# Performance work log

Measured on AMD Instinct MI355X. Metric: run time of the kernel, lower is better.

Reference implementation:

```python
import jax, jax.numpy as jnp
import numpy as np


def log_g(x):
    # torch: where(x>=0, log(relu(x)+0.5), -softplus(-x))
    return jnp.where(x >= 0, jnp.log(jnp.maximum(x, 0.0) + 0.5), -jax.nn.softplus(-x))


def parallel_scan_log(log_coeffs, log_values):
    # Faithful to source: cumsum over LAST (feature) dim, then pad time dim
    # (axis=1) with one leading zero row; logcumsumexp over time dim (axis=1).
    a_star = jnp.cumsum(log_coeffs, axis=-1)                      # [B,T,D]
    a_star = jnp.pad(a_star, ((0, 0), (1, 0), (0, 0)))            # [B,T+1,D]
    log_h0_plus_b_star = jax.lax.cumlogsumexp(log_values - a_star, axis=1)
    return jnp.exp(a_star + log_h0_plus_b_star)                   # [B,T+1,D]


def setup_inputs() -> dict:
    key = jax.random.key(0)
    ks = jax.random.split(key, 8)
    B, T, Din, Dout = 8, 4096, 1024, 1024
    scale = 1.0 / np.sqrt(Din)
    return {
        "x": jax.random.normal(ks[0], (B, T, Din), dtype=jnp.float32),
        "h_0": jax.random.uniform(ks[1], (B, 1, Dout), dtype=jnp.float32),
        "Wi": jax.random.uniform(ks[2], (Dout, Din), jnp.float32, -scale, scale),
        "bi": jax.random.uniform(ks[3], (Dout,), jnp.float32, -scale, scale),
        "Wf": jax.random.uniform(ks[4], (Dout, Din), jnp.float32, -scale, scale),
        "bf": jax.random.uniform(ks[5], (Dout,), jnp.float32, -scale, scale),
        "Wh": jax.random.uniform(ks[6], (Dout, Din), jnp.float32, -scale, scale),
        "bh": jax.random.uniform(ks[7], (Dout,), jnp.float32, -scale, scale),
    }


def reference(x, h_0, Wi, bi, Wf, bf, Wh, bh):
    # gate pre-activations: [B,T,Dout]
    zi = jnp.einsum('btd,od->bto', x, Wi) + bi
    zf = jnp.einsum('btd,od->bto', x, Wf) + bf
    zh = jnp.einsum('btd,od->bto', x, Wh) + bh
    diff = jax.nn.softplus(-zf) - jax.nn.softplus(-zi)
    log_f = -jax.nn.softplus(diff)
    log_i = -jax.nn.softplus(-diff)
    log_values = jnp.concatenate([log_g(h_0), log_i + log_g(zh)], axis=1)  # [B,T+1,D]
    return parallel_scan_log(log_f, log_values)
```

## Files before the change

### kernel.cpp

```cpp
#include <hip/hip_runtime.h>
#include <math.h>
#include <stdint.h>

#define B_    8
#define T_    4096
#define TP1   4097
#define D_    1024
#define K_    1024
#define M_    32768

#define BLK_M 128
#define BLK_N 64
#define BK    32

#define TC    64
#define NC    65

typedef __attribute__((ext_vector_type(8))) _Float16 f16x8;
typedef __attribute__((ext_vector_type(4))) float    f32x4;

__device__ __forceinline__ float sp_f(float x) {
    return fmaxf(x, 0.0f) + __logf(1.0f + __expf(-fabsf(x)));
}
__device__ __forceinline__ float log_g_f(float x) {
    return (x >= 0.0f) ? __logf(x + 0.5f) : x - __logf(1.0f + __expf(x));
}

__device__ __forceinline__ void g2lds16(const void* g, void* l) {
    __builtin_amdgcn_global_load_lds(
        (const __attribute__((address_space(1))) uint32_t*)g,
        (__attribute__((address_space(3))) uint32_t*)l,
        16, 0, 0);
}

__global__ __launch_bounds__(256) void k_cvt_x(
    const float* __restrict__ X, _Float16* __restrict__ Xs)
{
    int g = blockIdx.x * 256 + threadIdx.x;
    int l = g & 63;
    int frag = g >> 6;
    int kt = frag & 31;
    int mt = frag >> 5;
    int m = (mt << 4) + (l & 15);
    int k = (kt << 5) + ((l >> 4) << 3);
    const float4* p = (const float4*)&X[(size_t)m * K_ + k];
    float4 a = p[0], b = p[1];
    f16x8 h;
    h[0]=(_Float16)a.x; h[1]=(_Float16)a.y; h[2]=(_Float16)a.z; h[3]=(_Float16)a.w;
    h[4]=(_Float16)b.x; h[5]=(_Float16)b.y; h[6]=(_Float16)b.z; h[7]=(_Float16)b.w;
    *(f16x8*)&Xs[(size_t)g * 8] = h;
}

__global__ __launch_bounds__(256) void k_cvt_w(
    const float* __restrict__ Wi, const float* __restrict__ Wf,
    const float* __restrict__ Wh, _Float16* __restrict__ Ws)
{
    int g = blockIdx.x * 256 + threadIdx.x;
    int mat = g >> 17;
    int r = g & 131071;
    const float* W = (mat == 0) ? Wi : (mat == 1) ? Wf : Wh;
    int l = r & 63;
    int frag = r >> 6;
    int kt = frag & 31;
    int nt = frag >> 5;
    int n = (nt << 4) + (l & 15);
    int k = (kt << 5) + ((l >> 4) << 3);
    const float4* p = (const float4*)&W[(size_t)n * K_ + k];
    float4 a = p[0], b = p[1];
    f16x8 h;
    h[0]=(_Float16)a.x; h[1]=(_Float16)a.y; h[2]=(_Float16)a.z; h[3]=(_Float16)a.w;
    h[4]=(_Float16)b.x; h[5]=(_Float16)b.y; h[6]=(_Float16)b.z; h[7]=(_Float16)b.w;
    *(f16x8*)&Ws[(size_t)g * 8] = h;
}

__device__ __forceinline__ void stage_tile(
    const _Float16* Ag, const _Float16* Bg, int kt,
    _Float16* lAbuf, _Float16* lBbuf, int fa0, int fb0)
{
    g2lds16(Ag + (size_t)(fa0 * 32 + kt) * 512,       lAbuf + fa0 * 512);
    g2lds16(Ag + (size_t)((fa0 + 1) * 32 + kt) * 512, lAbuf + (fa0 + 1) * 512);
#pragma unroll
    for (int j = 0; j < 3; ++j) {
        int fb  = fb0 + j;
        int mat = fb >> 2, nf = fb & 3;
        g2lds16(Bg + ((size_t)mat * 2048 + (size_t)nf * 32 + kt) * 512,
                lBbuf + fb * 512);
    }
}

__device__ __forceinline__ void compute_tile(
    const _Float16* lAbuf, const _Float16* lBbuf,
    int wm, int wnf, int lane, f32x4 acc[3][4][2])
{
    f16x8 af[4];
#pragma unroll
    for (int mt = 0; mt < 4; ++mt)
        af[mt] = *(const f16x8*)&lAbuf[((wm >> 4) + mt) * 512 + lane * 8];
    __builtin_amdgcn_s_setprio(1);
#pragma unroll
    for (int a = 0; a < 3; ++a) {
#pragma unroll
        for (int nt = 0; nt < 2; ++nt) {
            f16x8 bfr = *(const f16x8*)&lBbuf[(a * 4 + wnf + nt) * 512 + lane * 8];
#pragma unroll
            for (int mt = 0; mt < 4; ++mt)
                acc[a][mt][nt] = __builtin_amdgcn_mfma_f32_16x16x32_f16(
                    af[mt], bfr, acc[a][mt][nt], 0, 0, 0);
        }
    }
    __builtin_amdgcn_s_setprio(0);
}

#define WAITBAR(N) do {                                         \
    asm volatile("s_waitcnt vmcnt(" #N ")" ::: "memory");       \
    __builtin_amdgcn_s_barrier();                               \
} while (0)

__global__ __launch_bounds__(256) void k_gemm(
    const _Float16* __restrict__ Xs, const _Float16* __restrict__ Ws,
    const float* __restrict__ bi, const float* __restrict__ bfv,
    const float* __restrict__ bh,
    float* __restrict__ ws_a, float* __restrict__ out)
{
    __shared__ __align__(16) _Float16 lA[3][8 * 512];
    __shared__ __align__(16) _Float16 lB[3][12 * 512];

    const int tid  = threadIdx.x;
    const int lane = tid & 63;
    const int w    = tid >> 6;

    const int bid = blockIdx.y * (int)gridDim.x + blockIdx.x;
    const int cpx = ((int)gridDim.x * (int)gridDim.y) >> 3;
    const int swz = (bid & 7) * cpx + (bid >> 3);
    const int n0  = (swz & 15) * BLK_N;
    const int m0  = (swz >> 4) * BLK_M;

    const int wm   = (w >> 1) * 64;
    const int wnf  = (w & 1) * 2;
    const int l16  = lane & 15;
    const int q    = lane >> 4;

    const int fa0 = w * 2;
    const int fb0 = w * 3;

    const _Float16* Ag = Xs + ((size_t)(m0 >> 4) * 32) * 512 + (size_t)lane * 8;
    const _Float16* Bg = Ws + (size_t)(n0 >> 4) * 32 * 512 + (size_t)lane * 8;

    f32x4 acc[3][4][2];
#pragma unroll
    for (int a = 0; a < 3; ++a)
#pragma unroll
        for (int mt = 0; mt < 4; ++mt)
#pragma unroll
            for (int nt = 0; nt < 2; ++nt) acc[a][mt][nt] = (f32x4)(0.0f);

    stage_tile(Ag, Bg, 0, lA[0], lB[0], fa0, fb0);
    stage_tile(Ag, Bg, 1, lA[1], lB[1], fa0, fb0);
    WAITBAR(5);

    for (int it = 0; it < 10; ++it) {
        const int kt = it * 3;

        stage_tile(Ag, Bg, kt + 2, lA[2], lB[2], fa0, fb0);
        compute_tile(lA[0], lB[0], wm, wnf, lane, acc);
        WAITBAR(5);

        stage_tile(Ag, Bg, kt + 3, lA[0], lB[0], fa0, fb0);
        compute_tile(lA[1], lB[1], wm, wnf, lane, acc);
        WAITBAR(5);

        stage_tile(Ag, Bg, kt + 4, lA[1], lB[1], fa0, fb0);
        compute_tile(lA[2], lB[2], wm, wnf, lane, acc);
        WAITBAR(5);
    }
    compute_tile(lA[0], lB[0], wm, wnf, lane, acc);
    WAITBAR(0);
    compute_tile(lA[1], lB[1], wm, wnf, lane, acc);

#pragma unroll
    for (int mt = 0; mt < 4; ++mt) {
#pragma unroll
        for (int nt = 0; nt < 2; ++nt) {
            int n = n0 + (wnf + nt) * 16 + l16;
            float biv = bi[n], bfvv = bfv[n], bhv = bh[n];
#pragma unroll
            for (int r = 0; r < 4; ++r) {
                int m = m0 + wm + mt * 16 + q * 4 + r;
                float zi = acc[0][mt][nt][r] + biv;
                float zf = acc[1][mt][nt][r] + bfvv;
                float zh = acc[2][mt][nt][r] + bhv;
                float spf = fmaxf(-zf, 0.0f) + __logf(1.0f + __expf(-fabsf(zf)));
                float spi = fmaxf(-zi, 0.0f) + __logf(1.0f + __expf(-fabsf(zi)));
                float df  = spf - spi;
                float spd = fmaxf(df, 0.0f) + __logf(1.0f + __expf(-fabsf(df)));
                float lf  = -spd;
                float li  = df - spd;
                float lg  = (zh >= 0.0f) ? __logf(zh + 0.5f)
                                         : zh - __logf(1.0f + __expf(zh));
                float lv  = li + lg;
                ws_a[(size_t)m * D_ + n] = lf;
                int b = m >> 12;
                out[(size_t)(m + b + 1) * D_ + n] = lv;
            }
        }
    }
}

__global__ __launch_bounds__(256) void k_cumsum(
    float* __restrict__ ws_a, float* __restrict__ out)
{
    const int tid  = threadIdx.x;
    const int lane = tid & 63;
    const int row  = blockIdx.x * 4 + (tid >> 6);
    const int b    = row >> 12;
    float* pa = ws_a + (size_t)row * D_;
    float* pu = out + (size_t)(row + b + 1) * D_;

    float vals[16];
#pragma unroll
    for (int j = 0; j < 4; ++j) {
        float4 v = *(const float4*)&pa[lane * 16 + j * 4];
        vals[j*4+0] = v.x; vals[j*4+1] = v.y; vals[j*4+2] = v.z; vals[j*4+3] = v.w;
    }
    float s = 0.0f;
#pragma unroll
    for (int j = 0; j < 16; ++j) s += vals[j];
    float inc = s;
#pragma unroll
    for (int off = 1; off < 64; off <<= 1) {
        float nv = __shfl_up(inc, off);
        if (lane >= off) inc += nv;
    }
    float run = inc - s;
#pragma unroll
    for (int j = 0; j < 16; ++j) { run += vals[j]; vals[j] = run; }
#pragma unroll
    for (int j = 0; j < 4; ++j) {
        float4 lv4 = *(const float4*)&pu[lane * 16 + j * 4];
        float4 a4; a4.x = vals[j*4]; a4.y = vals[j*4+1]; a4.z = vals[j*4+2]; a4.w = vals[j*4+3];
        float4 u4; u4.x = lv4.x - a4.x; u4.y = lv4.y - a4.y;
                   u4.z = lv4.z - a4.z; u4.w = lv4.w - a4.w;
        *(float4*)&pa[lane * 16 + j * 4] = a4;
        *(float4*)&pu[lane * 16 + j * 4] = u4;
    }
}

__global__ void k_h0(const float* __restrict__ h0, float* __restrict__ out)
{
    int i = blockIdx.x * 256 + threadIdx.x;
    int b = i >> 10, d = i & 1023;
    out[(size_t)b * TP1 * D_ + d] = log_g_f(h0[i]);
}

__global__ __launch_bounds__(256) void k_chunk(
    const float* __restrict__ out, float* __restrict__ ctm, float* __restrict__ cts)
{
    int c = blockIdx.x, b = blockIdx.y;
    int d = threadIdx.x * 4;
    int t0 = c * TC, t1 = min(TP1, t0 + TC);
    float4 m = make_float4(-__builtin_inff(), -__builtin_inff(),
                           -__builtin_inff(), -__builtin_inff());
    float4 s = make_float4(0.f, 0.f, 0.f, 0.f);
    const float* p = out + ((size_t)b * TP1 + t0) * D_ + d;
    for (int t = t0; t < t1; ++t) {
        float4 u = *(const float4*)p; p += D_;
        float4 mn;
        mn.x = fmaxf(m.x, u.x); mn.y = fmaxf(m.y, u.y);
        mn.z = fmaxf(m.z, u.z); mn.w = fmaxf(m.w, u.w);
        s.x = s.x * __expf(m.x - mn.x) + __expf(u.x - mn.x);
        s.y = s.y * __expf(m.y - mn.y) + __expf(u.y - mn.y);
        s.z = s.z * __expf(m.z - mn.z) + __expf(u.z - mn.z);
        s.w = s.w * __expf(m.w - mn.w) + __expf(u.w - mn.w);
        m = mn;
    }
    int ci = (b * NC + c) * D_ + d;
    *(float4*)&ctm[ci] = m; *(float4*)&cts[ci] = s;
}

__global__ __launch_bounds__(256) void k_carry(
    const float* __restrict__ ctm, const float* __restrict__ cts,
    float* __restrict__ carry)
{
    int i = blockIdx.x * 256 + threadIdx.x;
    int b = i >> 10, d = i & 1023;
    float m = -__builtin_inff(), s = 0.0f;
    for (int c = 0; c < NC; ++c) {
        int ci = (b * NC + c) * D_ + d;
        carry[ci] = (s == 0.0f) ? -__builtin_inff() : (m + __logf(s));
        float m2 = ctm[ci], s2 = cts[ci];
        float M = fmaxf(m, m2);
        s = s * __expf(m - M) + s2 * __expf(m2 - M);
        m = M;
    }
}

__global__ __launch_bounds__(256) void k_final(
    const float* __restrict__ ws_a, const float* __restrict__ carry,
    float* __restrict__ out)
{
    int c = blockIdx.x, b = blockIdx.y;
    int d = threadIdx.x * 4;
    int t0 = c * TC, t1 = min(TP1, t0 + TC);
    float4 v = *(const float4*)&carry[(b * NC + c) * D_ + d];
    float4 m, s;
    m.x = v.x; s.x = (v.x == -__builtin_inff()) ? 0.f : 1.f;
    m.y = v.y; s.y = (v.y == -__builtin_inff()) ? 0.f : 1.f;
    m.z = v.z; s.z = (v.z == -__builtin_inff()) ? 0.f : 1.f;
    m.w = v.w; s.w = (v.w == -__builtin_inff()) ? 0.f : 1.f;
    for (int t = t0; t < t1; ++t) {
        size_t oi = ((size_t)b * TP1 + t) * D_ + d;
        float4 u = *(const float4*)&out[oi];
        float4 mn;
        mn.x = fmaxf(m.x, u.x); mn.y = fmaxf(m.y, u.y);
        mn.z = fmaxf(m.z, u.z); mn.w = fmaxf(m.w, u.w);
        s.x = s.x * __expf(m.x - mn.x) + __expf(u.x - mn.x);
        s.y = s.y * __expf(m.y - mn.y) + __expf(u.y - mn.y);
        s.z = s.z * __expf(m.z - mn.z) + __expf(u.z - mn.z);
        s.w = s.w * __expf(m.w - mn.w) + __expf(u.w - mn.w);
        m = mn;
        float4 a = make_float4(0.f, 0.f, 0.f, 0.f);
        if (t != 0) a = *(const float4*)&ws_a[((size_t)b * T_ + (t - 1)) * D_ + d];
        float4 o;
        o.x = __expf(a.x + mn.x) * s.x;
        o.y = __expf(a.y + mn.y) * s.y;
        o.z = __expf(a.z + mn.z) * s.z;
        o.w = __expf(a.w + mn.w) * s.w;
        *(float4*)&out[oi] = o;
    }
}

extern "C" void kernel_launch(void* const* d_in, const int* in_sizes, int n_in,
                              void* d_out, int out_size, void* d_ws, size_t ws_size,
                              hipStream_t stream)
{
    const float* X   = (const float*)d_in[0];
    const float* h0  = (const float*)d_in[1];
    const float* Wi  = (const float*)d_in[2];
    const float* bi  = (const float*)d_in[3];
    const float* Wf  = (const float*)d_in[4];
    const float* bfv = (const float*)d_in[5];
    const float* Wh  = (const float*)d_in[6];
    const float* bh  = (const float*)d_in[7];
    float* out  = (float*)d_out;

    char* wsb = (char*)d_ws;
    float*    ws_a = (float*)wsb;
    _Float16* Xs   = (_Float16*)(wsb + (size_t)M_ * D_ * 4);
    _Float16* Wsv  = (_Float16*)(wsb + (size_t)M_ * D_ * 4 + (size_t)M_ * K_ * 2);
    float* ctm   = (float*)(wsb + (size_t)M_ * D_ * 4);
    float* cts   = ctm + B_ * NC * D_;
    float* carry = cts + B_ * NC * D_;

    k_cvt_x<<<M_ * K_ / 8 / 256, 256, 0, stream>>>(X, Xs);
    k_cvt_w<<<3 * D_ * K_ / 8 / 256, 256, 0, stream>>>(Wi, Wf, Wh, Wsv);

    dim3 g1(D_ / BLK_N, M_ / BLK_M);
    k_gemm<<<g1, 256, 0, stream>>>(Xs, Wsv, bi, bfv, bh, ws_a, out);
    k_h0<<<32, 256, 0, stream>>>(h0, out);
    k_cumsum<<<M_ / 4, 256, 0, stream>>>(ws_a, out);
    k_chunk<<<dim3(NC, B_), 256, 0, stream>>>(out, ctm, cts);
    k_carry<<<32, 256, 0, stream>>>(ctm, cts, carry);
    k_final<<<dim3(NC, B_), 256, 0, stream>>>(ws_a, carry, out);
}
```

Measured before the change: 804.6 us.

## Simplify gate log-math, merge conversion kernels, fold h0 into carry scan

The gate epilogue now computes log_f and log_i from two exponentials and three logs, using log(1+e^-zi)/(1+e^-zi + 1+e^-zf), instead of nested softplus calls. The two fp16 conversion kernels are merged into one launch, and the h0 row is handled inside the carry kernel, which seeds the scan so chunks align to 64 timesteps. The chunk kernel keeps two interleaved log-sum-exp accumulators to expose more instruction-level parallelism. The new form of the gate math may overflow in __expf for large negative pre-activations, a risk the softplus form avoided.

Result: faster. 763.8 us (-5.1%).

```diff
diff --git a/kernel.cpp b/kernel.cpp
--- a/kernel.cpp
+++ b/kernel.cpp
@@ -13,17 +13,20 @@
 #define BLK_N 64
 #define BK    32
 
-#define TC    64
-#define NC    65
+#define CH    64
+#define NCH   64
 
 typedef __attribute__((ext_vector_type(8))) _Float16 f16x8;
 typedef __attribute__((ext_vector_type(4))) float    f32x4;
 
-__device__ __forceinline__ float sp_f(float x) {
-    return fmaxf(x, 0.0f) + __logf(1.0f + __expf(-fabsf(x)));
-}
 __device__ __forceinline__ float log_g_f(float x) {
     return (x >= 0.0f) ? __logf(x + 0.5f) : x - __logf(1.0f + __expf(x));
+}
+
+__device__ __forceinline__ void lse_upd(float& m, float& s, float u) {
+    float mn = fmaxf(m, u);
+    s = s * __expf(m - mn) + __expf(u - mn);
+    m = mn;
 }
 
 __device__ __forceinline__ void g2lds16(const void* g, void* l) {
@@ -33,44 +36,44 @@
         16, 0, 0);
 }
 
-__global__ __launch_bounds__(256) void k_cvt_x(
-    const float* __restrict__ X, _Float16* __restrict__ Xs)
-{
-    int g = blockIdx.x * 256 + threadIdx.x;
-    int l = g & 63;
-    int frag = g >> 6;
-    int kt = frag & 31;
-    int mt = frag >> 5;
-    int m = (mt << 4) + (l & 15);
-    int k = (kt << 5) + ((l >> 4) << 3);
-    const float4* p = (const float4*)&X[(size_t)m * K_ + k];
-    float4 a = p[0], b = p[1];
-    f16x8 h;
-    h[0]=(_Float16)a.x; h[1]=(_Float16)a.y; h[2]=(_Float16)a.z; h[3]=(_Float16)a.w;
-    h[4]=(_Float16)b.x; h[5]=(_Float16)b.y; h[6]=(_Float16)b.z; h[7]=(_Float16)b.w;
-    *(f16x8*)&Xs[(size_t)g * 8] = h;
-}
-
-__global__ __launch_bounds__(256) void k_cvt_w(
-    const float* __restrict__ Wi, const float* __restrict__ Wf,
-    const float* __restrict__ Wh, _Float16* __restrict__ Ws)
-{
-    int g = blockIdx.x * 256 + threadIdx.x;
-    int mat = g >> 17;
-    int r = g & 131071;
-    const float* W = (mat == 0) ? Wi : (mat == 1) ? Wf : Wh;
-    int l = r & 63;
-    int frag = r >> 6;
-    int kt = frag & 31;
-    int nt = frag >> 5;
-    int n = (nt << 4) + (l & 15);
-    int k = (kt << 5) + ((l >> 4) << 3);
-    const float4* p = (const float4*)&W[(size_t)n * K_ + k];
-    float4 a = p[0], b = p[1];
-    f16x8 h;
-    h[0]=(_Float16)a.x; h[1]=(_Float16)a.y; h[2]=(_Float16)a.z; h[3]=(_Float16)a.w;
-    h[4]=(_Float16)b.x; h[5]=(_Float16)b.y; h[6]=(_Float16)b.z; h[7]=(_Float16)b.w;
-    *(f16x8*)&Ws[(size_t)g * 8] = h;
+__global__ __launch_bounds__(256) void k_cvt(
+    const float* __restrict__ X, const float* __restrict__ Wi,
+    const float* __restrict__ Wf, const float* __restrict__ Wh,
+    _Float16* __restrict__ Xs, _Float16* __restrict__ Ws)
+{
+    int bid = blockIdx.x;
+    if (bid < 1536) {
+        int g = bid * 256 + threadIdx.x;
+        int mat = g >> 17;
+        int r = g & 131071;
+        const float* W = (mat == 0) ? Wi : (mat == 1) ? Wf : Wh;
+        int l = r & 63;
+        int frag = r >> 6;
+        int kt = frag & 31;
+        int nt = frag >> 5;
+        int n = (nt << 4) + (l & 15);
+        int k = (kt << 5) + ((l >> 4) << 3);
+        const float4* p = (const float4*)&W[(size_t)n * K_ + k];
+        float4 a = p[0], b = p[1];
+        f16x8 h;
+        h[0]=(_Float16)a.x; h[1]=(_Float16)a.y; h[2]=(_Float16)a.z; h[3]=(_Float16)a.w;
+        h[4]=(_Float16)b.x; h[5]=(_Float16)b.y; h[6]=(_Float16)b.z; h[7]=(_Float16)b.w;
+        *(f16x8*)&Ws[(size_t)g * 8] = h;
+    } else {
+        int g = (bid - 1536) * 256 + threadIdx.x;
+        int l = g & 63;
+        int frag = g >> 6;
+        int kt = frag & 31;
+        int mt = frag >> 5;
+        int m = (mt << 4) + (l & 15);
+        int k = (kt << 5) + ((l >> 4) << 3);
+        const float4* p = (const float4*)&X[(size_t)m * K_ + k];
+        float4 a = p[0], b = p[1];
+        f16x8 h;
+        h[0]=(_Float16)a.x; h[1]=(_Float16)a.y; h[2]=(_Float16)a.z; h[3]=(_Float16)a.w;
+        h[4]=(_Float16)b.x; h[5]=(_Float16)b.y; h[6]=(_Float16)b.z; h[7]=(_Float16)b.w;
+        *(f16x8*)&Xs[(size_t)g * 8] = h;
+    }
 }
 
 __device__ __forceinline__ void stage_tile(
@@ -189,15 +192,14 @@
                 float zi = acc[0][mt][nt][r] + biv;
                 float zf = acc[1][mt][nt][r] + bfvv;
                 float zh = acc[2][mt][nt][r] + bhv;
-                float spf = fmaxf(-zf, 0.0f) + __logf(1.0f + __expf(-fabsf(zf)));
-                float spi = fmaxf(-zi, 0.0f) + __logf(1.0f + __expf(-fabsf(zi)));
-                float df  = spf - spi;
-                float spd = fmaxf(df, 0.0f) + __logf(1.0f + __expf(-fabsf(df)));
-                float lf  = -spd;
-                float li  = df - spd;
-                float lg  = (zh >= 0.0f) ? __logf(zh + 0.5f)
-                                         : zh - __logf(1.0f + __expf(zh));
-                float lv  = li + lg;
+                float ei = __expf(-zi), ef = __expf(-zf);
+                float Pi = 1.0f + ei,  Pf = 1.0f + ef;
+                float lS = __logf(Pi + Pf);
+                float lf = __logf(Pi) - lS;
+                float li = __logf(Pf) - lS;
+                float lg = (zh >= 0.0f) ? __logf(zh + 0.5f)
+                                        : zh - __logf(1.0f + __expf(zh));
+                float lv = li + lg;
                 ws_a[(size_t)m * D_ + n] = lf;
                 int b = m >> 12;
                 out[(size_t)(m + b + 1) * D_ + n] = lv;
@@ -245,25 +247,80 @@
     }
 }
 
-__global__ void k_h0(const float* __restrict__ h0, float* __restrict__ out)
+__global__ __launch_bounds__(256) void k_chunk(
+    const float* __restrict__ out, float* __restrict__ ctm, float* __restrict__ cts)
+{
+    int c = blockIdx.x, b = blockIdx.y;
+    int d = threadIdx.x * 4;
+    const float* p = out + ((size_t)b * TP1 + 1 + c * CH) * D_ + d;
+    float m0[4], s0[4], m1[4], s1[4];
+#pragma unroll
+    for (int e = 0; e < 4; ++e) {
+        m0[e] = -__builtin_inff(); s0[e] = 0.0f;
+        m1[e] = -__builtin_inff(); s1[e] = 0.0f;
+    }
+#pragma unroll 4
+    for (int i = 0; i < CH; i += 2) {
+        float4 ua = *(const float4*)(p + (size_t)i * D_);
+        float4 ub = *(const float4*)(p + (size_t)(i + 1) * D_);
+        lse_upd(m0[0], s0[0], ua.x); lse_upd(m0[1], s0[1], ua.y);
+        lse_upd(m0[2], s0[2], ua.z); lse_upd(m0[3], s0[3], ua.w);
+        lse_upd(m1[0], s1[0], ub.x); lse_upd(m1[1], s1[1], ub.y);
+        lse_upd(m1[2], s1[2], ub.z); lse_upd(m1[3], s1[3], ub.w);
+    }
+    size_t ci = ((size_t)b * NCH + c) * D_ + d;
+    float4 M4, S4;
+    {
+        float M, S;
+#define MERGE(e, dst_m, dst_s)                                        \
+        M = fmaxf(m0[e], m1[e]);                                      \
+        S = s0[e] * __expf(m0[e] - M) + s1[e] * __expf(m1[e] - M);    \
+        dst_m = M; dst_s = S;
+        MERGE(0, M4.x, S4.x); MERGE(1, M4.y, S4.y);
+        MERGE(2, M4.z, S4.z); MERGE(3, M4.w, S4.w);
+#undef MERGE
+    }
+    *(float4*)&ctm[ci] = M4;
+    *(float4*)&cts[ci] = S4;
+}
+
+__global__ __launch_bounds__(256) void k_carry(
+    const float* __restrict__ h0, const float* __restrict__ ctm,
+    const float* __restrict__ cts, float* __restrict__ carry,
+    float* __restrict__ out)
 {
     int i = blockIdx.x * 256 + threadIdx.x;
     int b = i >> 10, d = i & 1023;
-    out[(size_t)b * TP1 * D_ + d] = log_g_f(h0[i]);
-}
-
-__global__ __launch_bounds__(256) void k_chunk(
-    const float* __restrict__ out, float* __restrict__ ctm, float* __restrict__ cts)
+    float u0 = log_g_f(h0[i]);
+    out[(size_t)b * TP1 * D_ + d] = __expf(u0);
+    float m = u0, s = 1.0f;
+#pragma unroll 4
+    for (int c = 0; c < NCH; ++c) {
+        size_t ci = ((size_t)b * NCH + c) * D_ + d;
+        carry[ci] = m + __logf(s);
+        float m2 = ctm[ci], s2 = cts[ci];
+        float M = fmaxf(m, m2);
+        s = s * __expf(m - M) + s2 * __expf(m2 - M);
+        m = M;
+    }
+}
+
+__global__ __launch_bounds__(256) void k_final(
+    const float* __restrict__ ws_a, const float* __restrict__ carry,
+    float* __restrict__ out)
 {
     int c = blockIdx.x, b = blockIdx.y;
     int d = threadIdx.x * 4;
-    int t0 = c * TC, t1 = min(TP1, t0 + TC);
-    float4 m = make_float4(-__builtin_inff(), -__builtin_inff(),
-                           -__builtin_inff(), -__builtin_inff());
-    float4 s = make_float4(0.f, 0.f, 0.f, 0.f);
-    const float* p = out + ((size_t)b * TP1 + t0) * D_ + d;
-    for (int t = t0; t < t1; ++t) {
-        float4 u = *(const float4*)p; p += D_;
+    int t0 = 1 + c * CH;
+    float4 v = *(const float4*)&carry[((size_t)b * NCH + c) * D_ + d];
+    float4 m = v;
+    float4 s = make_float4(1.f, 1.f, 1.f, 1.f);
+#pragma unroll 2
+    for (int i = 0; i < CH; ++i) {
+        int t = t0 + i;
+        size_t oi = ((size_t)b * TP1 + t) * D_ + d;
+        float4 u = *(const float4*)&out[oi];
+        float4 a = *(const float4*)&ws_a[((size_t)b * T_ + (t - 1)) * D_ + d];
         float4 mn;
         mn.x = fmaxf(m.x, u.x); mn.y = fmaxf(m.y, u.y);
         mn.z = fmaxf(m.z, u.z); mn.w = fmaxf(m.w, u.w);
@@ -272,54 +329,6 @@
         s.z = s.z * __expf(m.z - mn.z) + __expf(u.z - mn.z);
         s.w = s.w * __expf(m.w - mn.w) + __expf(u.w - mn.w);
         m = mn;
-    }
-    int ci = (b * NC + c) * D_ + d;
-    *(float4*)&ctm[ci] = m; *(float4*)&cts[ci] = s;
-}
-
-__global__ __launch_bounds__(256) void k_carry(
-    const float* __restrict__ ctm, const float* __restrict__ cts,
-    float* __restrict__ carry)
-{
-    int i = blockIdx.x * 256 + threadIdx.x;
-    int b = i >> 10, d = i & 1023;
-    float m = -__builtin_inff(), s = 0.0f;
-    for (int c = 0; c < NC; ++c) {
-        int ci = (b * NC + c) * D_ + d;
-        carry[ci] = (s == 0.0f) ? -__builtin_inff() : (m + __logf(s));
-        float m2 = ctm[ci], s2 = cts[ci];
-        float M = fmaxf(m, m2);
-        s = s * __expf(m - M) + s2 * __expf(m2 - M);
-        m = M;
-    }
-}
-
-__global__ __launch_bounds__(256) void k_final(
-    const float* __restrict__ ws_a, const float* __restrict__ carry,
-    float* __restrict__ out)
-{
-    int c = blockIdx.x, b = blockIdx.y;
-    int d = threadIdx.x * 4;
-    int t0 = c * TC, t1 = min(TP1, t0 + TC);
-    float4 v = *(const float4*)&carry[(b * NC + c) * D_ + d];
-    float4 m, s;
-    m.x = v.x; s.x = (v.x == -__builtin_inff()) ? 0.f : 1.f;
-    m.y = v.y; s.y = (v.y == -__builtin_inff()) ? 0.f : 1.f;
-    m.z = v.z; s.z = (v.z == -__builtin_inff()) ? 0.f : 1.f;
-    m.w = v.w; s.w = (v.w == -__builtin_inff()) ? 0.f : 1.f;
-    for (int t = t0; t < t1; ++t) {
-        size_t oi = ((size_t)b * TP1 + t) * D_ + d;
-        float4 u = *(const float4*)&out[oi];
-        float4 mn;
-        mn.x = fmaxf(m.x, u.x); mn.y = fmaxf(m.y, u.y);
-        mn.z = fmaxf(m.z, u.z); mn.w = fmaxf(m.w, u.w);
-        s.x = s.x * __expf(m.x - mn.x) + __expf(u.x - mn.x);
-        s.y = s.y * __expf(m.y - mn.y) + __expf(u.y - mn.y);
-        s.z = s.z * __expf(m.z - mn.z) + __expf(u.z - mn.z);
-        s.w = s.w * __expf(m.w - mn.w) + __expf(u.w - mn.w);
-        m = mn;
-        float4 a = make_float4(0.f, 0.f, 0.f, 0.f);
-        if (t != 0) a = *(const float4*)&ws_a[((size_t)b * T_ + (t - 1)) * D_ + d];
         float4 o;
         o.x = __expf(a.x + mn.x) * s.x;
         o.y = __expf(a.y + mn.y) * s.y;
@@ -348,17 +357,15 @@
     _Float16* Xs   = (_Float16*)(wsb + (size_t)M_ * D_ * 4);
     _Float16* Wsv  = (_Float16*)(wsb + (size_t)M_ * D_ * 4 + (size_t)M_ * K_ * 2);
     float* ctm   = (float*)(wsb + (size_t)M_ * D_ * 4);
-    float* cts   = ctm + B_ * NC * D_;
-    float* carry = cts + B_ * NC * D_;
-
-    k_cvt_x<<<M_ * K_ / 8 / 256, 256, 0, stream>>>(X, Xs);
-    k_cvt_w<<<3 * D_ * K_ / 8 / 256, 256, 0, stream>>>(Wi, Wf, Wh, Wsv);
+    float* cts   = ctm + B_ * NCH * D_;
+    float* carry = cts + B_ * NCH * D_;
+
+    k_cvt<<<1536 + M_ * K_ / 8 / 256, 256, 0, stream>>>(X, Wi, Wf, Wh, Xs, Wsv);
 
     dim3 g1(D_ / BLK_N, M_ / BLK_M);
     k_gemm<<<g1, 256, 0, stream>>>(Xs, Wsv, bi, bfv, bh, ws_a, out);
-    k_h0<<<32, 256, 0, stream>>>(h0, out);
     k_cumsum<<<M_ / 4, 256, 0, stream>>>(ws_a, out);
-    k_chunk<<<dim3(NC, B_), 256, 0, stream>>>(out, ctm, cts);
-    k_carry<<<32, 256, 0, stream>>>(ctm, cts, carry);
-    k_final<<<dim3(NC, B_), 256, 0, stream>>>(ws_a, carry, out);
-}
+    k_chunk<<<dim3(NCH, B_), 256, 0, stream>>>(out, ctm, cts);
+    k_carry<<<32, 256, 0, stream>>>(h0, ctm, cts, carry, out);
+    k_final<<<dim3(NCH, B_), 256, 0, stream>>>(ws_a, carry, out);
+}
```
